# Kernel optimization log

Measured on AMD Instinct MI355X. Metric: run time of the kernel, lower is better.

The kernel has to match this reference:

```python
import jax, jax.numpy as jnp
import numpy as np

N_EMBD = 1024
N_HEAD = 16
EPS = 1e-5


def _layernorm(x, g, b):
    mu = jnp.mean(x, axis=-1, keepdims=True)
    var = jnp.mean(jnp.square(x - mu), axis=-1, keepdims=True)
    return (x - mu) * jax.lax.rsqrt(var + EPS) * g + b


def setup_inputs() -> dict:
    key = jax.random.key(0)
    ks = jax.random.split(key, 8)
    e = N_EMBD
    s = 0.02
    return {
        "x": jax.random.normal(ks[0], (4, 2048, e), dtype=jnp.float32),
        "ln1_g": jnp.ones((e,), jnp.float32),
        "ln1_b": jnp.zeros((e,), jnp.float32),
        "w_attn": jax.random.normal(ks[1], (e, 3 * e), jnp.float32) * s,
        "b_attn": jnp.zeros((3 * e,), jnp.float32),
        "w_proj": jax.random.normal(ks[2], (e, e), jnp.float32) * s,
        "b_proj": jnp.zeros((e,), jnp.float32),
        "ln2_g": jnp.ones((e,), jnp.float32),
        "ln2_b": jnp.zeros((e,), jnp.float32),
        "w_fc": jax.random.normal(ks[3], (e, 4 * e), jnp.float32) * s,
        "b_fc": jnp.zeros((4 * e,), jnp.float32),
        "w_fc2": jax.random.normal(ks[4], (4 * e, e), jnp.float32) * s,
        "b_fc2": jnp.zeros((e,), jnp.float32),
    }


def reference(x, ln1_g, ln1_b, w_attn, b_attn, w_proj, b_proj,
              ln2_g, ln2_b, w_fc, b_fc, w_fc2, b_fc2):
    b, s, e = x.shape
    h = N_HEAD
    d = e // h

    # --- attention sublayer (pre-LN) ---
    xn = _layernorm(x, ln1_g, ln1_b)
    qkv = xn @ w_attn + b_attn                      # [b, s, 3e]
    qkv = qkv.reshape(b, s, 3, h, d)
    q = jnp.transpose(qkv[:, :, 0], (0, 2, 1, 3))   # [b, h, s, d]
    k = jnp.transpose(qkv[:, :, 1], (0, 2, 1, 3))
    v = jnp.transpose(qkv[:, :, 2], (0, 2, 1, 3))

    mask = jnp.triu(jnp.ones((s, s), x.dtype), k=1) * jnp.asarray(-1e10, x.dtype)
    attn = jnp.einsum('bhqd,bhkd->bhqk', q, k) / jnp.sqrt(jnp.asarray(d, x.dtype))
    attn = jax.nn.softmax(attn + mask, axis=-1)
    out = jnp.einsum('bhqk,bhkd->bhqd', attn, v)    # [b, h, s, d]
    out = jnp.transpose(out, (0, 2, 1, 3)).reshape(b, s, e)
    x = x + (out @ w_proj + b_proj)

    # --- MLP sublayer (pre-LN) ---
    xn = _layernorm(x, ln2_g, ln2_b)
    hdn = jax.nn.gelu(xn @ w_fc + b_fc, approximate=False)
    x = x + (hdn @ w_fc2 + b_fc2)
    return x
```

## Files before the change

kernel.cpp:

```cpp
#include <hip/hip_runtime.h>

typedef unsigned short u16;
typedef unsigned int u32;
typedef __attribute__((ext_vector_type(8))) short bf16x8;
typedef __attribute__((ext_vector_type(4))) float f32x4;
typedef __attribute__((ext_vector_type(4))) u32 u32x4;

#define DEV __device__ __forceinline__
#define MFMA16(a, b, c) __builtin_amdgcn_mfma_f32_16x16x32_bf16(a, b, c, 0, 0, 0)

DEV u16 f2bf(float f) {
  u32 u = __float_as_uint(f);
  u32 r = (u + 0x7fffu + ((u >> 16) & 1u)) >> 16;
  return (u16)r;
}

DEV void async16(const void* g, void* l) {
  __builtin_amdgcn_global_load_lds((const __attribute__((address_space(1))) u32*)g,
                                   (__attribute__((address_space(3))) u32*)l, 16, 0, 0);
}

__global__ __launch_bounds__(256)
void wt_transpose(const float* __restrict__ w, u16* __restrict__ wt, int K, int N) {
  __shared__ float tile[32][33];
  int n0 = blockIdx.x * 32;
  int k0 = blockIdx.y * 32;
  int tx = threadIdx.x;
  int ty = threadIdx.y;
#pragma unroll
  for (int i = 0; i < 4; ++i)
    tile[ty + 8 * i][tx] = w[(size_t)(k0 + ty + 8 * i) * N + n0 + tx];
  __syncthreads();
#pragma unroll
  for (int i = 0; i < 4; ++i) {
    int n = ty + 8 * i;
    wt[(size_t)(n0 + n) * K + k0 + tx] = f2bf(tile[tx][n]);
  }
}

__global__ __launch_bounds__(256)
void ln_kernel(const float* __restrict__ x, const float* __restrict__ g,
               const float* __restrict__ b, u16* __restrict__ out) {
  int row = blockIdx.x;
  int tid = threadIdx.x;
  const float4* xr = (const float4*)(x + (size_t)row * 1024);
  float4 v = xr[tid];
  float s = v.x + v.y + v.z + v.w;
  float ss = v.x * v.x + v.y * v.y + v.z * v.z + v.w * v.w;
#pragma unroll
  for (int o = 32; o > 0; o >>= 1) {
    s += __shfl_down(s, o);
    ss += __shfl_down(ss, o);
  }
  __shared__ float ps[4], pss[4];
  if ((tid & 63) == 0) { ps[tid >> 6] = s; pss[tid >> 6] = ss; }
  __syncthreads();
  s = ps[0] + ps[1] + ps[2] + ps[3];
  ss = pss[0] + pss[1] + pss[2] + pss[3];
  float mu = s * (1.0f / 1024.0f);
  float var = ss * (1.0f / 1024.0f) - mu * mu;
  float rs = rsqrtf(var + 1e-5f);
  float4 gg = ((const float4*)g)[tid];
  float4 bb = ((const float4*)b)[tid];
  ushort4 ov;
  ov.x = f2bf((v.x - mu) * rs * gg.x + bb.x);
  ov.y = f2bf((v.y - mu) * rs * gg.y + bb.y);
  ov.z = f2bf((v.z - mu) * rs * gg.z + bb.z);
  ov.w = f2bf((v.w - mu) * rs * gg.w + bb.w);
  *(ushort4*)(out + (size_t)row * 1024 + tid * 4) = ov;
}

template <int EPI>
__global__ __launch_bounds__(256, 4)
void gemm128(const u16* __restrict__ A, const u16* __restrict__ Bt,
             const float* __restrict__ bias, int M, int N, int K,
             float* __restrict__ outf, u16* __restrict__ outb,
             const float* __restrict__ res,
             u16* __restrict__ qp, u16* __restrict__ kp, u16* __restrict__ vp) {
  __shared__ char lds[32768];
  const int tid = threadIdx.x;
  const int lane = tid & 63, wid = tid >> 6;
  const int wr = wid >> 1, wc = wid & 1;
  const int lr = lane & 15, hi = lane >> 4;
  const int swz = (lr & 7) << 4;

  const int nbx = gridDim.x;
  int lin = blockIdx.x + nbx * blockIdx.y;
  int xcd = lin & 7, j = lin >> 3;
  int bx = j % nbx;
  int by = xcd * 8 + j / nbx;

  const long m0 = (long)by * 128;
  const long n0 = (long)bx * 128;
  const long ldb = (long)K * 2;
  const char* Abase = (const char*)A + m0 * ldb;
  const char* Bbase = (const char*)Bt + n0 * ldb;

  f32x4 acc[4][4];
#pragma unroll
  for (int i = 0; i < 4; ++i)
#pragma unroll
    for (int jj = 0; jj < 4; ++jj) acc[i][jj] = (f32x4)0.0f;

  auto stage = [&](const char* base, int kt, int dst) {
#pragma unroll
    for (int l = 0; l < 4; ++l) {
      int c = (wid * 4 + l) * 64 + lane;
      int r = c >> 3, ch = c & 7;
      async16(base + (long)kt * 128 + (long)r * ldb + ((ch * 16) ^ ((r & 7) << 4)),
              lds + dst + (wid * 4 + l) * 1024);
    }
  };
  auto rdA = [&](int mi, int kk) {
    int rr = wr * 64 + mi * 16 + lr;
    return *(const bf16x8*)(lds + rr * 128 + ((kk * 64 + hi * 16) ^ swz));
  };
  auto rdB = [&](int ni, int kk) {
    int rr = wc * 64 + ni * 16 + lr;
    return *(const bf16x8*)(lds + 16384 + rr * 128 + ((kk * 64 + hi * 16) ^ swz));
  };

  const int NT = K >> 6;
  for (int kt = 0; kt < NT; ++kt) {
    stage(Abase, kt, 0);
    stage(Bbase, kt, 16384);
    __syncthreads();
#pragma unroll
    for (int kk = 0; kk < 2; ++kk) {
      bf16x8 a[4], b[4];
#pragma unroll
      for (int mi = 0; mi < 4; ++mi) a[mi] = rdA(mi, kk);
#pragma unroll
      for (int ni = 0; ni < 4; ++ni) b[ni] = rdB(ni, kk);
      __builtin_amdgcn_s_setprio(1);
#pragma unroll
      for (int mi = 0; mi < 4; ++mi)
#pragma unroll
        for (int ni = 0; ni < 4; ++ni)
          acc[mi][ni] = MFMA16(a[mi], b[ni], acc[mi][ni]);
      __builtin_amdgcn_s_setprio(0);
    }
    __syncthreads();
  }

  int rgrp = hi * 4;
#pragma unroll
  for (int mi = 0; mi < 4; ++mi) {
#pragma unroll
    for (int ni = 0; ni < 4; ++ni) {
      long col = n0 + wc * 64 + ni * 16 + lr;
      float bv = bias[col];
#pragma unroll
      for (int r = 0; r < 4; ++r) {
        long row = m0 + wr * 64 + mi * 16 + rgrp + r;
        float c = acc[mi][ni][r] + bv;
        if (EPI == 0) {
          int part = (int)(col >> 10);
          int hd = (int)(col & 1023);
          long bq = row >> 11;
          long sq = row & 2047;
          long bh = (bq << 4) + (hd >> 6);
          if (part == 0) {
            qp[(bh * 2048 + sq) * 64 + (hd & 63)] = f2bf(c * 0.18033688f);
          } else if (part == 1) {
            kp[(bh * 2048 + sq) * 64 + (hd & 63)] = f2bf(c);
          } else {
            vp[(bh << 17) + (long)(hd & 63) * 2048 + sq] = f2bf(c);
          }
        } else if (EPI == 1) {
          long idx = row * (long)N + col;
          outf[idx] = c + res[idx];
        } else {
          float t = c * (2.3022871f + 0.1029445f * c * c);
          float e = __builtin_amdgcn_exp2f(t);
          float gl = c - c / (e + 1.0f);
          outb[row * (long)N + col] = f2bf(gl);
        }
      }
    }
  }
}

__global__ __launch_bounds__(256, 2)
void attn_kernel(const u16* __restrict__ q, const u16* __restrict__ k,
                 const u16* __restrict__ vt, u16* __restrict__ outp) {
  __shared__ char ldsK[2][8192];
  __shared__ char ldsV[2][8192];
  __shared__ char ldsP[4][4096];
  int lin = blockIdx.x + 8 * blockIdx.y;
  int xcd = lin & 7, pos = lin >> 3;
  int j = pos >> 3;
  int bh = ((pos & 7) << 3) | xcd;
  int tid = threadIdx.x, lane = tid & 63, w = tid >> 6;
  const u16* qb = q + (size_t)bh * 131072;
  const u16* kb = k + (size_t)bh * 131072;
  const u16* vb = vt + (size_t)bh * 131072;

  int lr = lane & 15, lg = lane >> 4;
  int swz = (lr & 7) << 4;

  const int qih = 15 - j, qil = j;
  const int NTH = 2 * qih + 2;
  const int NTL = 2 * qil + 2;

  const bf16x8 ones = (bf16x8)(short)0x3F80;

  bf16x8 qf[2][2][2];
#pragma unroll
  for (int p = 0; p < 2; ++p) {
    int q0p = (p ? qil : qih) * 128;
#pragma unroll
    for (int fq = 0; fq < 2; ++fq) {
      const u16* qr = qb + (size_t)(q0p + w * 32 + fq * 16 + lr) * 64 + lg * 8;
      qf[p][fq][0] = *(const bf16x8*)(qr);
      qf[p][fq][1] = *(const bf16x8*)(qr + 32);
    }
  }

  f32x4 o[2][2][4];
  f32x4 lacc[2][2];
  float m_run[2][2][4];
#pragma unroll
  for (int p = 0; p < 2; ++p)
#pragma unroll
    for (int fq = 0; fq < 2; ++fq) {
      lacc[p][fq] = (f32x4)0.0f;
#pragma unroll
      for (int i = 0; i < 4; ++i) {
        o[p][fq][i] = (f32x4)0.0f;
        m_run[p][fq][i] = -1e30f;
      }
    }

  auto stage = [&](int buf, int t) {
    int kv0 = t * 64;
    const char* gk = (const char*)(kb + (size_t)kv0 * 64);
#pragma unroll
    for (int i = 0; i < 2; ++i) {
      int off = i * 4096 + tid * 16;
      int src = off ^ (((off >> 7) & 7) << 4);
      async16(gk + src, &ldsK[buf][i * 4096 + w * 1024]);
    }
#pragma unroll
    for (int i = 0; i < 2; ++i) {
      int vrow = i * 32 + (tid >> 3);
      int cb = ((tid & 7) * 16) ^ ((vrow & 7) << 4);
      async16((const char*)vb + (size_t)vrow * 4096 + (size_t)kv0 * 2 + cb,
              &ldsV[buf][i * 4096 + w * 1024]);
    }
  };

  stage(0, 0);
  __syncthreads();
  int cur = 0;

  for (int t = 0; t < NTH; ++t) {
    if (t + 1 < NTH) stage(cur ^ 1, t + 1);
    int kv0 = t * 64;

#pragma unroll
    for (int p = 0; p < 2; ++p) {
      if (p == 1 && t >= NTL) break;
      int q0p = (p ? qil : qih) * 128;
      int ntp = p ? NTL : NTH;

      f32x4 s[2][4];
      __builtin_amdgcn_s_setprio(1);
#pragma unroll
      for (int nf = 0; nf < 4; ++nf) {
#pragma unroll
        for (int fq = 0; fq < 2; ++fq) s[fq][nf] = (f32x4)0.0f;
#pragma unroll
        for (int ks = 0; ks < 2; ++ks) {
          bf16x8 kf = *(const bf16x8*)(&ldsK[cur][(nf * 16 + lr) * 128 +
                                                 ((ks * 64 + lg * 16) ^ swz)]);
#pragma unroll
          for (int fq = 0; fq < 2; ++fq)
            s[fq][nf] = MFMA16(qf[p][fq][ks], kf, s[fq][nf]);
        }
      }
      __builtin_amdgcn_s_setprio(0);

      if (t + 2 >= ntp) {
#pragma unroll
        for (int fq = 0; fq < 2; ++fq)
#pragma unroll
          for (int nf = 0; nf < 4; ++nf)
#pragma unroll
            for (int r = 0; r < 4; ++r) {
              int qrow = q0p + w * 32 + fq * 16 + lg * 4 + r;
              int kvc = kv0 + nf * 16 + lr;
              if (kvc > qrow) s[fq][nf][r] = -1e30f;
            }
      }

      float pmx[2][4];
      bool need = false;
#pragma unroll
      for (int fq = 0; fq < 2; ++fq)
#pragma unroll
        for (int r = 0; r < 4; ++r) {
          pmx[fq][r] = fmaxf(fmaxf(s[fq][0][r], s[fq][1][r]),
                             fmaxf(s[fq][2][r], s[fq][3][r]));
          need = need || (pmx[fq][r] > m_run[p][fq][r] + 11.5f);
        }
      if (__any(need)) {
#pragma unroll
        for (int fq = 0; fq < 2; ++fq)
#pragma unroll
          for (int r = 0; r < 4; ++r) {
            float pm = pmx[fq][r];
#pragma unroll
            for (int m = 1; m < 16; m <<= 1) pm = fmaxf(pm, __shfl_xor(pm, m));
            float mnew = fmaxf(m_run[p][fq][r], pm);
            float al = __builtin_amdgcn_exp2f(m_run[p][fq][r] - mnew);
            m_run[p][fq][r] = mnew;
            lacc[p][fq][r] *= al;
#pragma unroll
            for (int nf = 0; nf < 4; ++nf) o[p][fq][nf][r] *= al;
          }
      }

#pragma unroll
      for (int fq = 0; fq < 2; ++fq)
#pragma unroll
        for (int nf = 0; nf < 4; ++nf)
#pragma unroll
          for (int r = 0; r < 4; ++r) {
            float pv = __builtin_amdgcn_exp2f(s[fq][nf][r] - m_run[p][fq][r]);
            int prow = fq * 16 + lg * 4 + r;
            int pb = ((nf * 16 + lr) * 2) ^ ((prow & 7) << 4);
            *(u16*)(&ldsP[w][prow * 128 + pb]) = (u16)(__float_as_uint(pv) >> 16);
          }

      __builtin_amdgcn_s_setprio(1);
#pragma unroll
      for (int ks = 0; ks < 2; ++ks) {
        bf16x8 pf[2];
#pragma unroll
        for (int fq = 0; fq < 2; ++fq)
          pf[fq] = *(const bf16x8*)(&ldsP[w][(fq * 16 + lr) * 128 +
                                             ((ks * 64 + lg * 16) ^ swz)]);
        lacc[p][0] = MFMA16(pf[0], ones, lacc[p][0]);
        lacc[p][1] = MFMA16(pf[1], ones, lacc[p][1]);
#pragma unroll
        for (int nf = 0; nf < 4; ++nf) {
          bf16x8 vf = *(const bf16x8*)(&ldsV[cur][(nf * 16 + lr) * 128 +
                                                 ((ks * 64 + lg * 16) ^ swz)]);
#pragma unroll
          for (int fq = 0; fq < 2; ++fq)
            o[p][fq][nf] = MFMA16(pf[fq], vf, o[p][fq][nf]);
        }
      }
      __builtin_amdgcn_s_setprio(0);
    }

    __syncthreads();
    cur ^= 1;
  }

  int b = bh >> 4, h = bh & 15;
#pragma unroll
  for (int p = 0; p < 2; ++p) {
    int q0p = (p ? qil : qih) * 128;
#pragma unroll
    for (int fq = 0; fq < 2; ++fq)
#pragma unroll
      for (int r = 0; r < 4; ++r) {
        int qrow = q0p + w * 32 + fq * 16 + lg * 4 + r;
        float inv = 1.0f / lacc[p][fq][r];
        size_t base = ((size_t)(b * 2048 + qrow)) * 1024 + h * 64;
#pragma unroll
        for (int nf = 0; nf < 4; ++nf)
          outp[base + nf * 16 + lr] = f2bf(o[p][fq][nf][r] * inv);
      }
  }
}

extern "C" void kernel_launch(void* const* d_in, const int* in_sizes, int n_in,
                              void* d_out, int out_size, void* d_ws, size_t ws_size,
                              hipStream_t stream) {
  const float* x      = (const float*)d_in[0];
  const float* ln1_g  = (const float*)d_in[1];
  const float* ln1_b  = (const float*)d_in[2];
  const float* w_attn = (const float*)d_in[3];
  const float* b_attn = (const float*)d_in[4];
  const float* w_proj = (const float*)d_in[5];
  const float* b_proj = (const float*)d_in[6];
  const float* ln2_g  = (const float*)d_in[7];
  const float* ln2_b  = (const float*)d_in[8];
  const float* w_fc   = (const float*)d_in[9];
  const float* b_fc   = (const float*)d_in[10];
  const float* w_fc2  = (const float*)d_in[11];
  const float* b_fc2  = (const float*)d_in[12];
  float* out = (float*)d_out;

  char* ws = (char*)d_ws;
  u16* wt_attn = (u16*)(ws + 0);
  u16* wt_proj = (u16*)(ws + 6291456);
  u16* wt_fc   = (u16*)(ws + 8388608);
  u16* wt_fc2  = (u16*)(ws + 16777216);
  u16* xn      = (u16*)(ws + 25165824);
  float* x2    = (float*)(ws + 41943040);
  char* region = ws + 75497472;
  u16* qb = (u16*)(region);
  u16* kb = (u16*)(region + 16777216);
  u16* vt = (u16*)(region + 33554432);
  u16* ao = (u16*)(region + 50331648);
  u16* hm = (u16*)(region);

  dim3 tb(32, 8);
  wt_transpose<<<dim3(3072 / 32, 1024 / 32), tb, 0, stream>>>(w_attn, wt_attn, 1024, 3072);
  wt_transpose<<<dim3(1024 / 32, 1024 / 32), tb, 0, stream>>>(w_proj, wt_proj, 1024, 1024);
  wt_transpose<<<dim3(4096 / 32, 1024 / 32), tb, 0, stream>>>(w_fc, wt_fc, 1024, 4096);
  wt_transpose<<<dim3(1024 / 32, 4096 / 32), tb, 0, stream>>>(w_fc2, wt_fc2, 4096, 1024);

  ln_kernel<<<8192, 256, 0, stream>>>(x, ln1_g, ln1_b, xn);

  gemm128<0><<<dim3(3072 / 128, 8192 / 128), 256, 0, stream>>>(
      xn, wt_attn, b_attn, 8192, 3072, 1024,
      nullptr, nullptr, nullptr, qb, kb, vt);

  attn_kernel<<<dim3(8, 64), 256, 0, stream>>>(qb, kb, vt, ao);

  gemm128<1><<<dim3(1024 / 128, 8192 / 128), 256, 0, stream>>>(
      ao, wt_proj, b_proj, 8192, 1024, 1024,
      x2, nullptr, x, nullptr, nullptr, nullptr);

  ln_kernel<<<8192, 256, 0, stream>>>(x2, ln2_g, ln2_b, xn);

  gemm128<2><<<dim3(4096 / 128, 8192 / 128), 256, 0, stream>>>(
      xn, wt_fc, b_fc, 8192, 4096, 1024,
      nullptr, hm, nullptr, nullptr, nullptr, nullptr);

  gemm128<1><<<dim3(1024 / 128, 8192 / 128), 256, 0, stream>>>(
      hm, wt_fc2, b_fc2, 8192, 1024, 4096,
      out, nullptr, x2, nullptr, nullptr, nullptr);
}
```

Baseline: 369.3 us.

## Halve attention query tile to 64 rows, doubling grid and occupancy

The attention kernel now has each workgroup handle two 64-row query tiles, one wave per 16 rows, where it previously handled two 128-row tiles. The grid doubles to 16x64 blocks and launch bounds ask for 4 blocks per CU. The P scratch buffer and register arrays shrink to match, and the causal mask now applies only on the diagonal tile. This trades K/V reuse per block, since each staged K/V tile now feeds half as many query rows, for more parallelism and occupancy.

```diff
diff --git a/kernel.cpp b/kernel.cpp
--- a/kernel.cpp
+++ b/kernel.cpp
@@ -181,13 +181,13 @@
   }
 }
 
-__global__ __launch_bounds__(256, 2)
+__global__ __launch_bounds__(256, 4)
 void attn_kernel(const u16* __restrict__ q, const u16* __restrict__ k,
                  const u16* __restrict__ vt, u16* __restrict__ outp) {
   __shared__ char ldsK[2][8192];
   __shared__ char ldsV[2][8192];
-  __shared__ char ldsP[4][4096];
-  int lin = blockIdx.x + 8 * blockIdx.y;
+  __shared__ char ldsP[4][2048];
+  int lin = blockIdx.x + 16 * blockIdx.y;
   int xcd = lin & 7, pos = lin >> 3;
   int j = pos >> 3;
   int bh = ((pos & 7) << 3) | xcd;
@@ -199,38 +199,33 @@
   int lr = lane & 15, lg = lane >> 4;
   int swz = (lr & 7) << 4;
 
-  const int qih = 15 - j, qil = j;
-  const int NTH = 2 * qih + 2;
-  const int NTL = 2 * qil + 2;
+  const int qih = 31 - j, qil = j;
+  const int NTH = qih + 1;
+  const int NTL = qil + 1;
 
   const bf16x8 ones = (bf16x8)(short)0x3F80;
 
-  bf16x8 qf[2][2][2];
+  bf16x8 qf[2][2];
 #pragma unroll
   for (int p = 0; p < 2; ++p) {
-    int q0p = (p ? qil : qih) * 128;
-#pragma unroll
-    for (int fq = 0; fq < 2; ++fq) {
-      const u16* qr = qb + (size_t)(q0p + w * 32 + fq * 16 + lr) * 64 + lg * 8;
-      qf[p][fq][0] = *(const bf16x8*)(qr);
-      qf[p][fq][1] = *(const bf16x8*)(qr + 32);
-    }
-  }
-
-  f32x4 o[2][2][4];
-  f32x4 lacc[2][2];
-  float m_run[2][2][4];
-#pragma unroll
-  for (int p = 0; p < 2; ++p)
-#pragma unroll
-    for (int fq = 0; fq < 2; ++fq) {
-      lacc[p][fq] = (f32x4)0.0f;
-#pragma unroll
-      for (int i = 0; i < 4; ++i) {
-        o[p][fq][i] = (f32x4)0.0f;
-        m_run[p][fq][i] = -1e30f;
-      }
-    }
+    int q0p = (p ? qil : qih) * 64;
+    const u16* qr = qb + (size_t)(q0p + w * 16 + lr) * 64 + lg * 8;
+    qf[p][0] = *(const bf16x8*)(qr);
+    qf[p][1] = *(const bf16x8*)(qr + 32);
+  }
+
+  f32x4 o[2][4];
+  f32x4 lacc[2];
+  float m_run[2][4];
+#pragma unroll
+  for (int p = 0; p < 2; ++p) {
+    lacc[p] = (f32x4)0.0f;
+#pragma unroll
+    for (int i = 0; i < 4; ++i) {
+      o[p][i] = (f32x4)0.0f;
+      m_run[p][i] = -1e30f;
+    }
+  }
 
   auto stage = [&](int buf, int t) {
     int kv0 = t * 64;
@@ -261,95 +256,77 @@
 #pragma unroll
     for (int p = 0; p < 2; ++p) {
       if (p == 1 && t >= NTL) break;
-      int q0p = (p ? qil : qih) * 128;
+      int q0p = (p ? qil : qih) * 64;
       int ntp = p ? NTL : NTH;
 
-      f32x4 s[2][4];
+      f32x4 s[4];
       __builtin_amdgcn_s_setprio(1);
 #pragma unroll
       for (int nf = 0; nf < 4; ++nf) {
-#pragma unroll
-        for (int fq = 0; fq < 2; ++fq) s[fq][nf] = (f32x4)0.0f;
+        s[nf] = (f32x4)0.0f;
 #pragma unroll
         for (int ks = 0; ks < 2; ++ks) {
           bf16x8 kf = *(const bf16x8*)(&ldsK[cur][(nf * 16 + lr) * 128 +
                                                  ((ks * 64 + lg * 16) ^ swz)]);
-#pragma unroll
-          for (int fq = 0; fq < 2; ++fq)
-            s[fq][nf] = MFMA16(qf[p][fq][ks], kf, s[fq][nf]);
+          s[nf] = MFMA16(qf[p][ks], kf, s[nf]);
         }
       }
       __builtin_amdgcn_s_setprio(0);
 
-      if (t + 2 >= ntp) {
-#pragma unroll
-        for (int fq = 0; fq < 2; ++fq)
-#pragma unroll
-          for (int nf = 0; nf < 4; ++nf)
-#pragma unroll
-            for (int r = 0; r < 4; ++r) {
-              int qrow = q0p + w * 32 + fq * 16 + lg * 4 + r;
-              int kvc = kv0 + nf * 16 + lr;
-              if (kvc > qrow) s[fq][nf][r] = -1e30f;
-            }
-      }
-
-      float pmx[2][4];
+      if (t + 1 == ntp) {
+#pragma unroll
+        for (int nf = 0; nf < 4; ++nf)
+#pragma unroll
+          for (int r = 0; r < 4; ++r) {
+            int qrow = q0p + w * 16 + lg * 4 + r;
+            int kvc = kv0 + nf * 16 + lr;
+            if (kvc > qrow) s[nf][r] = -1e30f;
+          }
+      }
+
+      float pmx[4];
       bool need = false;
 #pragma unroll
-      for (int fq = 0; fq < 2; ++fq)
+      for (int r = 0; r < 4; ++r) {
+        pmx[r] = fmaxf(fmaxf(s[0][r], s[1][r]), fmaxf(s[2][r], s[3][r]));
+        need = need || (pmx[r] > m_run[p][r] + 11.5f);
+      }
+      if (__any(need)) {
 #pragma unroll
         for (int r = 0; r < 4; ++r) {
-          pmx[fq][r] = fmaxf(fmaxf(s[fq][0][r], s[fq][1][r]),
-                             fmaxf(s[fq][2][r], s[fq][3][r]));
-          need = need || (pmx[fq][r] > m_run[p][fq][r] + 11.5f);
+          float pm = pmx[r];
+#pragma unroll
+          for (int m = 1; m < 16; m <<= 1) pm = fmaxf(pm, __shfl_xor(pm, m));
+          float mnew = fmaxf(m_run[p][r], pm);
+          float al = __builtin_amdgcn_exp2f(m_run[p][r] - mnew);
+          m_run[p][r] = mnew;
+          lacc[p][r] *= al;
+#pragma unroll
+          for (int nf = 0; nf < 4; ++nf) o[p][nf][r] *= al;
         }
-      if (__any(need)) {
-#pragma unroll
-        for (int fq = 0; fq < 2; ++fq)
-#pragma unroll
-          for (int r = 0; r < 4; ++r) {
-            float pm = pmx[fq][r];
-#pragma unroll
-            for (int m = 1; m < 16; m <<= 1) pm = fmaxf(pm, __shfl_xor(pm, m));
-            float mnew = fmaxf(m_run[p][fq][r], pm);
-            float al = __builtin_amdgcn_exp2f(m_run[p][fq][r] - mnew);
-            m_run[p][fq][r] = mnew;
-            lacc[p][fq][r] *= al;
-#pragma unroll
-            for (int nf = 0; nf < 4; ++nf) o[p][fq][nf][r] *= al;
-          }
-      }
-
-#pragma unroll
-      for (int fq = 0; fq < 2; ++fq)
-#pragma unroll
-        for (int nf = 0; nf < 4; ++nf)
-#pragma unroll
-          for (int r = 0; r < 4; ++r) {
-            float pv = __builtin_amdgcn_exp2f(s[fq][nf][r] - m_run[p][fq][r]);
-            int prow = fq * 16 + lg * 4 + r;
-            int pb = ((nf * 16 + lr) * 2) ^ ((prow & 7) << 4);
-            *(u16*)(&ldsP[w][prow * 128 + pb]) = (u16)(__float_as_uint(pv) >> 16);
-          }
+      }
+
+#pragma unroll
+      for (int nf = 0; nf < 4; ++nf)
+#pragma unroll
+        for (int r = 0; r < 4; ++r) {
+          float pv = __builtin_amdgcn_exp2f(s[nf][r] - m_run[p][r]);
+          int prow = lg * 4 + r;
+          int pb = ((nf * 16 + lr) * 2) ^ ((prow & 7) << 4);
+          *(u16*)(&ldsP[w][prow * 128 + pb]) = (u16)(__float_as_uint(pv) >> 16);
+        }
 
       __builtin_amdgcn_s_setprio(1);
 #pragma unroll
       for (int ks = 0; ks < 2; ++ks) {
-        bf16x8 pf[2];
-#pragma unroll
-        for (int fq = 0; fq < 2; ++fq)
-          pf[fq] = *(const bf16x8*)(&ldsP[w][(fq * 16 + lr) * 128 +
+        bf16x8 pf = *(const bf16x8*)(&ldsP[w][lr * 128 +
                                              ((ks * 64 + lg * 16) ^ swz)]);
-        lacc[p][0] = MFMA16(pf[0], ones, lacc[p][0]);
-        lacc[p][1] = MFMA16(pf[1], ones, lacc[p][1]);
+        lacc[p] = MFMA16(pf, ones, lacc[p]);
 #pragma unroll
         for (int nf = 0; nf < 4; ++nf) {
           bf16x8 vf = *(const bf16x8*)(&ldsV[cur][(nf * 16 + lr) * 128 +
                                                  ((ks * 64 + lg * 16) ^ swz)]);
-#pragma unroll
-          for (int fq = 0; fq < 2; ++fq)
-            o[p][fq][nf] = MFMA16(pf[fq], vf, o[p][fq][nf]);
+          o[p][nf] = MFMA16(pf, vf, o[p][nf]);
         }
       }
       __builtin_amdgcn_s_setprio(0);
@@ -362,18 +339,16 @@
   int b = bh >> 4, h = bh & 15;
 #pragma unroll
   for (int p = 0; p < 2; ++p) {
-    int q0p = (p ? qil : qih) * 128;
-#pragma unroll
-    for (int fq = 0; fq < 2; ++fq)
-#pragma unroll
-      for (int r = 0; r < 4; ++r) {
-        int qrow = q0p + w * 32 + fq * 16 + lg * 4 + r;
-        float inv = 1.0f / lacc[p][fq][r];
-        size_t base = ((size_t)(b * 2048 + qrow)) * 1024 + h * 64;
-#pragma unroll
-        for (int nf = 0; nf < 4; ++nf)
-          outp[base + nf * 16 + lr] = f2bf(o[p][fq][nf][r] * inv);
-      }
+    int q0p = (p ? qil : qih) * 64;
+#pragma unroll
+    for (int r = 0; r < 4; ++r) {
+      int qrow = q0p + w * 16 + lg * 4 + r;
+      float inv = 1.0f / lacc[p][r];
+      size_t base = ((size_t)(b * 2048 + qrow)) * 1024 + h * 64;
+#pragma unroll
+      for (int nf = 0; nf < 4; ++nf)
+        outp[base + nf * 16 + lr] = f2bf(o[p][nf][r] * inv);
+    }
   }
 }
 
@@ -421,7 +396,7 @@
       xn, wt_attn, b_attn, 8192, 3072, 1024,
       nullptr, nullptr, nullptr, qb, kb, vt);
 
-  attn_kernel<<<dim3(8, 64), 256, 0, stream>>>(qb, kb, vt, ao);
+  attn_kernel<<<dim3(16, 64), 256, 0, stream>>>(qb, kb, vt, ao);
 
   gemm128<1><<<dim3(1024 / 128, 8192 / 128), 256, 0, stream>>>(
       ao, wt_proj, b_proj, 8192, 1024, 1024,
```

Result: no change. 371.2 us (+0.5%).
